# Performance work log

Hardware: AMD Instinct MI355X
Metric: run time of the kernel (lower is better)

The kernel has to match this reference:

```python
import jax, jax.numpy as jnp
import numpy as np

N_QUBITS = 10
DIM = 2 ** N_QUBITS
W_MUL = (2 ** 0.5) * 5 ** (-0.5)  # he_std * lrmul with gain=sqrt(2), use_wscale=True, lrmul=1
C64 = jnp.complex64


def _rx(t):
    c = jnp.cos(t / 2).astype(C64)
    s = (-1j * jnp.sin(t / 2)).astype(C64)
    return jnp.stack([jnp.stack([c, s]), jnp.stack([s, c])])


def _ry(t):
    c = jnp.cos(t / 2).astype(C64)
    s = jnp.sin(t / 2).astype(C64)
    return jnp.stack([jnp.stack([c, -s]), jnp.stack([s, c])])


def _rz(t):
    e0 = jnp.exp(-1j * t.astype(C64) / 2)
    e1 = jnp.exp(1j * t.astype(C64) / 2)
    z = jnp.zeros((), C64)
    return jnp.stack([jnp.stack([e0, z]), jnp.stack([z, e1])])


def _apply_1q(U, g, q, n):
    # left-multiply full gate (I x g x I) @ U without materializing the kron
    U = U.reshape(2 ** q, 2, -1)  # (pre, qubit, rest*cols)
    U = jnp.einsum('ab,xby->xay', g, U)
    return U.reshape(2 ** n, 2 ** n)


def _apply_cnot(U, c, t, n):
    # left-multiply CNOT(control=c, target=t) @ U; qubit 0 is most significant
    dim = 2 ** n
    T = U.reshape((2,) * n + (-1,))
    flipped = jnp.flip(T, axis=t)  # X on target
    res = jnp.stack([jnp.take(T, 0, axis=c), jnp.take(flipped, 1, axis=c)], axis=c)
    return res.reshape(dim, dim)


def _circuit_unitary(w, n):
    U = jnp.eye(2 ** n, dtype=C64)
    for q in range(n):
        U = _apply_1q(U, _rx(w[6 * q + 0]), q, n)
        U = _apply_1q(U, _ry(w[6 * q + 1]), q, n)
        U = _apply_1q(U, _rz(w[6 * q + 2]), q, n)
    for q in range(n - 1):
        U = _apply_cnot(U, q, q + 1, n)
    U = _apply_cnot(U, n - 1, 0, n)
    for q in range(n):
        U = _apply_1q(U, _rx(w[6 * q + 3]), q, n)
        U = _apply_1q(U, _ry(w[6 * q + 4]), q, n)
        U = _apply_1q(U, _rz(w[6 * q + 5]), q, n)
    return U


def _ptrace(rho, dA, dB):
    # trace out the second subsystem: (dA,dB,dA,dB) -> (dA,dA)
    return jnp.einsum('ibjb->ij', rho.reshape(dA, dB, dA, dB))


def setup_inputs() -> dict:
    key = jax.random.key(0)
    k1, k2, k3 = jax.random.split(key, 3)
    inputA = jax.random.normal(k1, (32, 32), dtype=jnp.float32)
    inputB = jax.random.normal(k2, (32, 32), dtype=jnp.float32)
    weight = jax.random.uniform(k3, (6 * N_QUBITS,), minval=0.0,
                                maxval=2 * np.pi, dtype=jnp.float32)
    return {"inputA": inputA, "inputB": inputB, "weight": weight,
            "dimA": 32, "dimB": 32}


def reference(inputA, inputB, weight, dimA, dimB):
    w = weight * W_MUL
    U = _circuit_unitary(w, N_QUBITS)
    Ud = U.conj().T
    A = inputA.astype(C64)
    B = inputB.astype(C64)
    rhoAB = jnp.kron(A, B)
    U_AB = U @ rhoAB @ Ud
    rhoBA = jnp.kron(B, A)
    U_BA = U @ rhoBA @ Ud
    mutualBatA = _ptrace(U_AB, dimA, dimB)
    mutualAatB = _ptrace(U_BA, dimB, dimA)
    return (mutualBatA, mutualAatB)
```

## Files before the change

kernel.cpp:

```cpp
#include <hip/hip_runtime.h>

#define WMUL 0.63245553203367586640f

typedef float v2f __attribute__((ext_vector_type(2)));
typedef float v4f __attribute__((ext_vector_type(4)));

__device__ __forceinline__ v4f cat(v2f a, v2f b) { return __builtin_shufflevector(a, b, 0, 1, 2, 3); }
__device__ __forceinline__ v2f lo2(v4f t) { return __builtin_shufflevector(t, t, 0, 1); }
__device__ __forceinline__ v2f hi2(v4f t) { return __builtin_shufflevector(t, t, 2, 3); }

__device__ __forceinline__ v2f cmul_c(v2f a, v2f b) {
    v2f r = { a.x*b.x - a.y*b.y, a.x*b.y + a.y*b.x };
    return r;
}
__device__ __forceinline__ v2f cmacc_c(v2f acc, v2f a, v2f b) {
    acc.x += a.x*b.x - a.y*b.y;
    acc.y += a.x*b.y + a.y*b.x;
    return acc;
}

__device__ __forceinline__ void cmacc_pk(v2f& d, v2f a, v2f b) {
    asm("v_pk_fma_f32 %0, %1, %2, %0 op_sel_hi:[0,1,1]\n\t"
        "v_pk_fma_f32 %0, %1, %2, %0 op_sel:[1,1,0] op_sel_hi:[1,0,1] neg_lo:[1,0,0]"
        : "+v"(d) : "v"(a), "v"(b));
}
__device__ __forceinline__ void cmacc_cj_pk(v2f& d, v2f a, v2f b) {
    asm("v_pk_fma_f32 %0, %1, %2, %0 op_sel_hi:[0,1,1]\n\t"
        "v_pk_fma_f32 %0, %1, %2, %0 op_sel:[1,1,0] op_sel_hi:[1,0,1] neg_hi:[1,0,0]"
        : "+v"(d) : "v"(a), "v"(b));
}
__device__ __forceinline__ void cmacc_rj_pk(v2f& d, v2f a, v2f m) {
    asm("v_pk_fma_f32 %0, %1, %2, %0 neg_hi:[1,0,0]"
        : "+v"(d) : "v"(a), "v"(m));
}

__global__ __launch_bounds__(256)
void qmutual_kernel(const float* __restrict__ A, const float* __restrict__ B,
                    const float* __restrict__ weight, float* __restrict__ out,
                    int out_size)
{
    __shared__ __align__(16) v2f arena[7360];
    v2f* CLA   = arena;
    v2f* CLB   = arena + 1024;
    v2f* CL2A  = arena + 2048;
    v2f* TAT   = arena + 3072;
    v2f* TBT   = arena + 4160;
    v2f* A1p   = arena + 5248;
    v2f* B1p   = arena + 6304;
    v2f* Sarr  = arena + 3072;
    v2f* Np    = arena;
    v2f* TFT   = arena + 3072;
    v2f* gates = arena + 5248;

    const int tid = threadIdx.x;
    const int i0 = tid >> 4, j0 = tid & 15;
    const int r0 = 2*i0, c0 = 2*j0;
    const int blk = blockIdx.x;
    const float* MA = blk ? B : A;
    const float* MB = blk ? A : B;

    if (tid < 20) {
        const int layer = tid / 10, q = tid % 10;
        const float w0 = weight[6*q + 3*layer + 0] * WMUL;
        const float w1 = weight[6*q + 3*layer + 1] * WMUL;
        const float w2 = weight[6*q + 3*layer + 2] * WMUL;
        const float cx = cosf(0.5f*w0), sx = sinf(0.5f*w0);
        const float cy = cosf(0.5f*w1), sy = sinf(0.5f*w1);
        const float cz = cosf(0.5f*w2), sz = sinf(0.5f*w2);
        v2f rx[2][2] = { { {cx,0.f}, {0.f,-sx} }, { {0.f,-sx}, {cx,0.f} } };
        v2f ry[2][2] = { { {cy,0.f}, {-sy,0.f} }, { {sy,0.f}, {cy,0.f} } };
        const v2f rz0 = {cz, -sz}, rz1 = {cz, sz};
        v2f m[2][2];
        #pragma unroll
        for (int r = 0; r < 2; ++r)
            #pragma unroll
            for (int c = 0; c < 2; ++c)
                m[r][c] = cmacc_c(cmul_c(ry[r][0], rx[0][c]), ry[r][1], rx[1][c]);
        v2f* g = gates + tid*4;
        g[0] = cmul_c(rz0, m[0][0]); g[1] = cmul_c(rz0, m[0][1]);
        g[2] = cmul_c(rz1, m[1][0]); g[3] = cmul_c(rz1, m[1][1]);
    }
    __syncthreads();

    {
        v2f vals[3][2][2];
        #pragma unroll
        for (int mat = 0; mat < 3; ++mat) {
            const int gbase = (mat == 0) ? 0 : (mat == 1 ? 5 : 10);
            #pragma unroll
            for (int kk = 0; kk < 2; ++kk)
                #pragma unroll
                for (int jj = 0; jj < 2; ++jj) {
                    const int k = r0 + kk, j = c0 + jj;
                    v2f v = {1.f, 0.f};
                    #pragma unroll
                    for (int q = 0; q < 5; ++q) {
                        const int rb = (j >> (4-q)) & 1;
                        const int cb = (k >> (4-q)) & 1;
                        v = cmul_c(v, gates[(gbase+q)*4 + rb*2 + cb]);
                    }
                    v2f cv = { v.x, -v.y };
                    vals[mat][kk][jj] = cv;
                }
        }
        #pragma unroll
        for (int kk = 0; kk < 2; ++kk) {
            *(v4f*)&CLA [(r0+kk)*32 + c0] = cat(vals[0][kk][0], vals[0][kk][1]);
            *(v4f*)&CLB [(r0+kk)*32 + c0] = cat(vals[1][kk][0], vals[1][kk][1]);
            *(v4f*)&CL2A[(r0+kk)*32 + c0] = cat(vals[2][kk][0], vals[2][kk][1]);
        }
    }
    __syncthreads();

    {
        v2f ta[2][2] = {}, tb[2][2] = {};
        #pragma unroll
        for (int k = 0; k < 32; ++k) {
            const v4f xa = *(const v4f*)&CLA[k*32 + r0];
            const v4f xb = *(const v4f*)&CLB[k*32 + r0];
            const float2 ma = *(const float2*)&MA[k*32 + c0];
            const float2 mb = *(const float2*)&MB[k*32 + c0];
            const v2f xa0 = lo2(xa), xa1 = hi2(xa);
            const v2f xb0 = lo2(xb), xb1 = hi2(xb);
            const v2f mx = {ma.x, ma.x}, my = {ma.y, ma.y};
            const v2f nx = {mb.x, mb.x}, ny = {mb.y, mb.y};
            cmacc_rj_pk(ta[0][0], xa0, mx); cmacc_rj_pk(ta[0][1], xa0, my);
            cmacc_rj_pk(ta[1][0], xa1, mx); cmacc_rj_pk(ta[1][1], xa1, my);
            cmacc_rj_pk(tb[0][0], xb0, nx); cmacc_rj_pk(tb[0][1], xb0, ny);
            cmacc_rj_pk(tb[1][0], xb1, nx); cmacc_rj_pk(tb[1][1], xb1, ny);
        }
        #pragma unroll
        for (int g = 0; g < 2; ++g) {
            *(v4f*)&TAT[(c0+g)*34 + r0] = cat(ta[0][g], ta[1][g]);
            *(v4f*)&TBT[(c0+g)*34 + r0] = cat(tb[0][g], tb[1][g]);
        }
    }
    __syncthreads();

    {
        v2f a1[2][2] = {}, b1[2][2] = {};
        #pragma unroll
        for (int k = 0; k < 32; ++k) {
            const v4f t  = *(const v4f*)&TAT[k*34 + r0];
            const v4f u  = *(const v4f*)&TBT[k*34 + r0];
            const v4f ca = *(const v4f*)&CLA[k*32 + c0];
            const v4f cb = *(const v4f*)&CLB[k*32 + c0];
            const v2f t0 = lo2(t), t1 = hi2(t), u0 = lo2(u), u1 = hi2(u);
            const v2f ca0 = lo2(ca), ca1 = hi2(ca), cb0 = lo2(cb), cb1 = hi2(cb);
            cmacc_pk(a1[0][0], t0, ca0); cmacc_pk(a1[0][1], t0, ca1);
            cmacc_pk(a1[1][0], t1, ca0); cmacc_pk(a1[1][1], t1, ca1);
            cmacc_pk(b1[0][0], u0, cb0); cmacc_pk(b1[0][1], u0, cb1);
            cmacc_pk(b1[1][0], u1, cb0); cmacc_pk(b1[1][1], u1, cb1);
        }
        #pragma unroll
        for (int p = 0; p < 2; ++p)
            #pragma unroll
            for (int g = 0; g < 2; ++g) {
                A1p[(r0+p)*33 + c0+g] = a1[p][g];
                B1p[(r0+p)*33 + c0+g] = b1[p][g];
            }
    }
    __syncthreads();

    if (tid < 8) {
        const int p = (tid >> 2) & 1, eps = (tid >> 1) & 1, del = tid & 1;
        v2f s = {0.f, 0.f};
        #pragma unroll
        for (int m = 0; m < 16; ++m) {
            const int kb = 2*m + p;
            const int g  = kb ^ (kb >> 1);
            s += B1p[((eps<<4)^g)*33 + ((del<<4)^g)];
        }
        Sarr[tid] = s;
    }
    __syncthreads();

    {
        const int gr0 = r0 ^ (r0 >> 1), gr1 = (r0+1) ^ ((r0+1) >> 1);
        const int gc0 = c0 ^ (c0 >> 1), gc1 = (c0+1) ^ ((c0+1) >> 1);
        const v2f A00 = A1p[gr0*33 + gc0],        A01 = A1p[gr0*33 + gc1];
        const v2f A10 = A1p[gr1*33 + gc0],        A11 = A1p[gr1*33 + gc1];
        const v2f X00 = A1p[(gr0^24)*33 + (gc0^24)], X01 = A1p[(gr0^24)*33 + (gc1^24)];
        const v2f X10 = A1p[(gr1^24)*33 + (gc0^24)], X11 = A1p[(gr1^24)*33 + (gc1^24)];
        v2f n[2][2] = {};
        cmacc_pk(n[0][0], A00, Sarr[0]); cmacc_pk(n[0][0], X00, Sarr[4]);
        cmacc_pk(n[0][1], A01, Sarr[1]); cmacc_pk(n[0][1], X01, Sarr[5]);
        cmacc_pk(n[1][0], A10, Sarr[2]); cmacc_pk(n[1][0], X10, Sarr[6]);
        cmacc_pk(n[1][1], A11, Sarr[3]); cmacc_pk(n[1][1], X11, Sarr[7]);
        #pragma unroll
        for (int p = 0; p < 2; ++p)
            *(v4f*)&Np[(r0+p)*34 + c0] = cat(n[p][0], n[p][1]);
    }
    __syncthreads();

    {
        v2f tf[2][2] = {};
        #pragma unroll
        for (int k = 0; k < 32; ++k) {
            const v4f x = *(const v4f*)&CL2A[k*32 + r0];
            const v4f m = *(const v4f*)&Np[k*34 + c0];
            const v2f x0 = lo2(x), x1 = hi2(x), m0 = lo2(m), m1 = hi2(m);
            cmacc_cj_pk(tf[0][0], x0, m0); cmacc_cj_pk(tf[0][1], x0, m1);
            cmacc_cj_pk(tf[1][0], x1, m0); cmacc_cj_pk(tf[1][1], x1, m1);
        }
        #pragma unroll
        for (int g = 0; g < 2; ++g)
            *(v4f*)&TFT[(c0+g)*34 + r0] = cat(tf[0][g], tf[1][g]);
    }
    __syncthreads();

    {
        v2f rr[2][2] = {};
        #pragma unroll
        for (int k = 0; k < 32; ++k) {
            const v4f t  = *(const v4f*)&TFT[k*34 + r0];
            const v4f c2 = *(const v4f*)&CL2A[k*32 + c0];
            const v2f t0 = lo2(t), t1 = hi2(t), c20 = lo2(c2), c21 = hi2(c2);
            cmacc_pk(rr[0][0], t0, c20); cmacc_pk(rr[0][1], t0, c21);
            cmacc_pk(rr[1][0], t1, c20); cmacc_pk(rr[1][1], t1, c21);
        }
        if (out_size >= 4096) {
            #pragma unroll
            for (int p = 0; p < 2; ++p)
                *(v4f*)&out[blk*2048 + (r0+p)*64 + 4*j0] = cat(rr[p][0], rr[p][1]);
        } else {
            #pragma unroll
            for (int p = 0; p < 2; ++p) {
                float2 v = { rr[p][0].x, rr[p][1].x };
                *(float2*)&out[blk*1024 + (r0+p)*32 + c0] = v;
            }
        }
    }
}

extern "C" void kernel_launch(void* const* d_in, const int* in_sizes, int n_in,
                              void* d_out, int out_size, void* d_ws, size_t ws_size,
                              hipStream_t stream) {
    const float* A = (const float*)d_in[0];
    const float* B = (const float*)d_in[1];
    const float* w = (const float*)d_in[2];
    float* out = (float*)d_out;
    qmutual_kernel<<<2, 256, 0, stream>>>(A, B, w, out, out_size);
}
```

Baseline: 66.75 us.

## Factor gate kron products and compute only needed B-side trace entries

```diff
diff --git a/kernel.cpp b/kernel.cpp
--- a/kernel.cpp
+++ b/kernel.cpp
@@ -31,6 +31,10 @@
 }
 __device__ __forceinline__ void cmacc_rj_pk(v2f& d, v2f a, v2f m) {
     asm("v_pk_fma_f32 %0, %1, %2, %0 neg_hi:[1,0,0]"
+        : "+v"(d) : "v"(a), "v"(m));
+}
+__device__ __forceinline__ void cmacc_r_pk(v2f& d, v2f a, v2f m) {
+    asm("v_pk_fma_f32 %0, %1, %2, %0"
         : "+v"(d) : "v"(a), "v"(m));
 }
 
@@ -44,13 +48,16 @@
     v2f* CLB   = arena + 1024;
     v2f* CL2A  = arena + 2048;
     v2f* TAT   = arena + 3072;
-    v2f* TBT   = arena + 4160;
+    v2f* W     = arena + 4160;
     v2f* A1p   = arena + 5248;
-    v2f* B1p   = arena + 6304;
     v2f* Sarr  = arena + 3072;
     v2f* Np    = arena;
     v2f* TFT   = arena + 3072;
     v2f* gates = arena + 5248;
+    v2f* Pb    = arena + 6304;
+    v2f* Rb    = arena + 6352;
+    v2f* Qb    = arena + 6400;
+    v2f* ent   = arena + 6304;
 
     const int tid = threadIdx.x;
     const int i0 = tid >> 4, j0 = tid & 15;
@@ -59,7 +66,7 @@
     const float* MA = blk ? B : A;
     const float* MB = blk ? A : B;
 
-    if (tid < 20) {
+    if (tid < 15) {
         const int layer = tid / 10, q = tid % 10;
         const float w0 = weight[6*q + 3*layer + 0] * WMUL;
         const float w1 = weight[6*q + 3*layer + 1] * WMUL;
@@ -82,83 +89,103 @@
     }
     __syncthreads();
 
-    {
-        v2f vals[3][2][2];
-        #pragma unroll
-        for (int mat = 0; mat < 3; ++mat) {
-            const int gbase = (mat == 0) ? 0 : (mat == 1 ? 5 : 10);
-            #pragma unroll
-            for (int kk = 0; kk < 2; ++kk)
-                #pragma unroll
-                for (int jj = 0; jj < 2; ++jj) {
-                    const int k = r0 + kk, j = c0 + jj;
-                    v2f v = {1.f, 0.f};
-                    #pragma unroll
-                    for (int q = 0; q < 5; ++q) {
-                        const int rb = (j >> (4-q)) & 1;
-                        const int cb = (k >> (4-q)) & 1;
-                        v = cmul_c(v, gates[(gbase+q)*4 + rb*2 + cb]);
-                    }
-                    v2f cv = { v.x, -v.y };
-                    vals[mat][kk][jj] = cv;
-                }
-        }
-        #pragma unroll
-        for (int kk = 0; kk < 2; ++kk) {
-            *(v4f*)&CLA [(r0+kk)*32 + c0] = cat(vals[0][kk][0], vals[0][kk][1]);
-            *(v4f*)&CLB [(r0+kk)*32 + c0] = cat(vals[1][kk][0], vals[1][kk][1]);
-            *(v4f*)&CL2A[(r0+kk)*32 + c0] = cat(vals[2][kk][0], vals[2][kk][1]);
-        }
-    }
-    __syncthreads();
-
-    {
-        v2f ta[2][2] = {}, tb[2][2] = {};
+    if (tid < 48) {
+        const int m = tid >> 4, idx = tid & 15;
+        const int jh = idx >> 2, kh = idx & 3;
+        Pb[m*16 + idx] = cmul_c(gates[(5*m+0)*4 + (jh>>1)*2 + (kh>>1)],
+                                gates[(5*m+1)*4 + (jh&1)*2 + (kh&1)]);
+    } else if (tid < 96) {
+        const int t = tid - 48, m = t >> 4, idx = t & 15;
+        const int jm = idx >> 2, km = idx & 3;
+        Rb[m*16 + idx] = cmul_c(gates[(5*m+2)*4 + (jm>>1)*2 + (km>>1)],
+                                gates[(5*m+3)*4 + (jm&1)*2 + (km&1)]);
+    }
+    __syncthreads();
+
+    if (tid < 192) {
+        const int m = tid >> 6, idx = tid & 63;
+        const int jl = idx >> 3, kl = idx & 7;
+        Qb[m*64 + idx] = cmul_c(Rb[m*16 + (jl>>1)*4 + (kl>>1)],
+                                gates[(5*m+4)*4 + (jl&1)*2 + (kl&1)]);
+    }
+    __syncthreads();
+
+    {
+        const int jh = c0 >> 3, kh = r0 >> 3, jl0 = c0 & 7, kl0 = r0 & 7;
+        v2f* dst[3] = { CLA, CLB, CL2A };
+        #pragma unroll
+        for (int m = 0; m < 3; ++m) {
+            const v2f Pv = Pb[m*16 + jh*4 + kh];
+            const v4f q0 = *(const v4f*)&Qb[m*64 + jl0*8 + kl0];
+            const v4f q1 = *(const v4f*)&Qb[m*64 + (jl0+1)*8 + kl0];
+            const v2f v00 = cmul_c(Pv, lo2(q0));
+            const v2f v10 = cmul_c(Pv, hi2(q0));
+            const v2f v01 = cmul_c(Pv, lo2(q1));
+            const v2f v11 = cmul_c(Pv, hi2(q1));
+            const v2f n00 = {v00.x, -v00.y}, n01 = {v01.x, -v01.y};
+            const v2f n10 = {v10.x, -v10.y}, n11 = {v11.x, -v11.y};
+            *(v4f*)&dst[m][(r0  )*32 + c0] = cat(n00, n01);
+            *(v4f*)&dst[m][(r0+1)*32 + c0] = cat(n10, n11);
+        }
+    }
+    __syncthreads();
+
+    {
+        v2f ta[2][2] = {}, w[2][2] = {};
         #pragma unroll
         for (int k = 0; k < 32; ++k) {
             const v4f xa = *(const v4f*)&CLA[k*32 + r0];
-            const v4f xb = *(const v4f*)&CLB[k*32 + r0];
             const float2 ma = *(const float2*)&MA[k*32 + c0];
-            const float2 mb = *(const float2*)&MB[k*32 + c0];
+            const v4f cb = *(const v4f*)&CLB[k*32 + c0];
+            const float mb0 = MB[r0*32 + k], mb1 = MB[(r0+1)*32 + k];
             const v2f xa0 = lo2(xa), xa1 = hi2(xa);
-            const v2f xb0 = lo2(xb), xb1 = hi2(xb);
+            const v2f cb0 = lo2(cb), cb1 = hi2(cb);
             const v2f mx = {ma.x, ma.x}, my = {ma.y, ma.y};
-            const v2f nx = {mb.x, mb.x}, ny = {mb.y, mb.y};
+            const v2f m0 = {mb0, mb0},  m1 = {mb1, mb1};
             cmacc_rj_pk(ta[0][0], xa0, mx); cmacc_rj_pk(ta[0][1], xa0, my);
             cmacc_rj_pk(ta[1][0], xa1, mx); cmacc_rj_pk(ta[1][1], xa1, my);
-            cmacc_rj_pk(tb[0][0], xb0, nx); cmacc_rj_pk(tb[0][1], xb0, ny);
-            cmacc_rj_pk(tb[1][0], xb1, nx); cmacc_rj_pk(tb[1][1], xb1, ny);
-        }
-        #pragma unroll
-        for (int g = 0; g < 2; ++g) {
+            cmacc_r_pk(w[0][0], cb0, m0); cmacc_r_pk(w[0][1], cb1, m0);
+            cmacc_r_pk(w[1][0], cb0, m1); cmacc_r_pk(w[1][1], cb1, m1);
+        }
+        #pragma unroll
+        for (int g = 0; g < 2; ++g)
             *(v4f*)&TAT[(c0+g)*34 + r0] = cat(ta[0][g], ta[1][g]);
-            *(v4f*)&TBT[(c0+g)*34 + r0] = cat(tb[0][g], tb[1][g]);
-        }
-    }
-    __syncthreads();
-
-    {
-        v2f a1[2][2] = {}, b1[2][2] = {};
+        #pragma unroll
+        for (int p = 0; p < 2; ++p)
+            *(v4f*)&W[(r0+p)*34 + c0] = cat(w[p][0], w[p][1]);
+    }
+    __syncthreads();
+
+    {
+        v2f a1[2][2] = {};
         #pragma unroll
         for (int k = 0; k < 32; ++k) {
             const v4f t  = *(const v4f*)&TAT[k*34 + r0];
-            const v4f u  = *(const v4f*)&TBT[k*34 + r0];
             const v4f ca = *(const v4f*)&CLA[k*32 + c0];
-            const v4f cb = *(const v4f*)&CLB[k*32 + c0];
-            const v2f t0 = lo2(t), t1 = hi2(t), u0 = lo2(u), u1 = hi2(u);
-            const v2f ca0 = lo2(ca), ca1 = hi2(ca), cb0 = lo2(cb), cb1 = hi2(cb);
+            const v2f t0 = lo2(t), t1 = hi2(t);
+            const v2f ca0 = lo2(ca), ca1 = hi2(ca);
             cmacc_pk(a1[0][0], t0, ca0); cmacc_pk(a1[0][1], t0, ca1);
             cmacc_pk(a1[1][0], t1, ca0); cmacc_pk(a1[1][1], t1, ca1);
-            cmacc_pk(b1[0][0], u0, cb0); cmacc_pk(b1[0][1], u0, cb1);
-            cmacc_pk(b1[1][0], u1, cb0); cmacc_pk(b1[1][1], u1, cb1);
         }
         #pragma unroll
         for (int p = 0; p < 2; ++p)
             #pragma unroll
-            for (int g = 0; g < 2; ++g) {
+            for (int g = 0; g < 2; ++g)
                 A1p[(r0+p)*33 + c0+g] = a1[p][g];
-                B1p[(r0+p)*33 + c0+g] = b1[p][g];
-            }
+
+        const int e = tid >> 1, h = tid & 1;
+        const int kb = e >> 2, eps = (e >> 1) & 1, del = e & 1;
+        const int gg = kb ^ (kb >> 1);
+        const int rB = (eps << 4) ^ gg, cB = (del << 4) ^ gg;
+        v2f acc = {0.f, 0.f};
+        #pragma unroll
+        for (int i = 0; i < 16; ++i) {
+            const int k = 16*h + i;
+            cmacc_cj_pk(acc, CLB[k*32 + rB], W[k*34 + cB]);
+        }
+        acc.x += __shfl_xor(acc.x, 1);
+        acc.y += __shfl_xor(acc.y, 1);
+        if (h == 0) ent[e] = acc;
     }
     __syncthreads();
 
@@ -166,11 +193,8 @@
         const int p = (tid >> 2) & 1, eps = (tid >> 1) & 1, del = tid & 1;
         v2f s = {0.f, 0.f};
         #pragma unroll
-        for (int m = 0; m < 16; ++m) {
-            const int kb = 2*m + p;
-            const int g  = kb ^ (kb >> 1);
-            s += B1p[((eps<<4)^g)*33 + ((del<<4)^g)];
-        }
+        for (int m = 0; m < 16; ++m)
+            s += ent[(2*m + p)*4 + eps*2 + del];
         Sarr[tid] = s;
     }
     __syncthreads();
@@ -178,8 +202,8 @@
     {
         const int gr0 = r0 ^ (r0 >> 1), gr1 = (r0+1) ^ ((r0+1) >> 1);
         const int gc0 = c0 ^ (c0 >> 1), gc1 = (c0+1) ^ ((c0+1) >> 1);
-        const v2f A00 = A1p[gr0*33 + gc0],        A01 = A1p[gr0*33 + gc1];
-        const v2f A10 = A1p[gr1*33 + gc0],        A11 = A1p[gr1*33 + gc1];
+        const v2f A00 = A1p[gr0*33 + gc0],           A01 = A1p[gr0*33 + gc1];
+        const v2f A10 = A1p[gr1*33 + gc0],           A11 = A1p[gr1*33 + gc1];
         const v2f X00 = A1p[(gr0^24)*33 + (gc0^24)], X01 = A1p[(gr0^24)*33 + (gc1^24)];
         const v2f X10 = A1p[(gr1^24)*33 + (gc0^24)], X11 = A1p[(gr1^24)*33 + (gc1^24)];
         v2f n[2][2] = {};
@@ -203,6 +227,7 @@
             cmacc_cj_pk(tf[0][0], x0, m0); cmacc_cj_pk(tf[0][1], x0, m1);
             cmacc_cj_pk(tf[1][0], x1, m0); cmacc_cj_pk(tf[1][1], x1, m1);
         }
+        __syncthreads();
         #pragma unroll
         for (int g = 0; g < 2; ++g)
             *(v4f*)&TFT[(c0+g)*34 + r0] = cat(tf[0][g], tf[1][g]);
```

New measurement: 67.16 us. About the same (+0.6%).
